# Optimization experiments

Measured on AMD Instinct MI355X. Metric: run time of the kernel, lower is better.

## Reference

```python
import jax, jax.numpy as jnp
import numpy as np
from math import lgamma, pi, sqrt

L = 20  # legendre_polys; embedding_dim = L*L = 400
SQ2 = sqrt(2.0)

def _norm(l, m):
    # K(l,m) = sqrt((2l+1)/(4pi) * (l-m)!/(l+m)!), computed stably via lgamma
    return sqrt((2 * l + 1) / (4.0 * pi)) * sqrt(np.exp(lgamma(l - m + 1) - lgamma(l + m + 1)))

def setup_inputs() -> dict:
    key = jax.random.key(0)
    k1, k2 = jax.random.split(key)
    B = 250000
    lon = jax.random.uniform(k1, (B,), minval=-180.0, maxval=180.0)
    lat = jax.random.uniform(k2, (B,), minval=-90.0, maxval=90.0)
    return {"lonlat": jnp.stack([lon, lat], axis=-1).astype(jnp.float32)}

def _sh_all(lonlat):
    # Real spherical harmonics for all (l, m), l in [0, L), m in [-l, l],
    # in the same ordering as the torch module's double loop.
    lon, lat = lonlat[:, 0], lonlat[:, 1]
    phi = jnp.deg2rad(lon + 180.0)    # azimuth in [0, 2pi)
    theta = jnp.deg2rad(lat + 90.0)   # colatitude in [0, pi]
    x = jnp.cos(theta)
    sx = jnp.sin(theta)               # = sqrt(1 - x^2) on [0, pi]

    # Associated Legendre P_l^m(x) (Condon-Shortley phase) via recurrence.
    P = {(0, 0): jnp.ones_like(x)}
    for m in range(1, L):
        P[(m, m)] = -(2 * m - 1) * sx * P[(m - 1, m - 1)]
    for m in range(L):
        if m + 1 < L:
            P[(m + 1, m)] = (2 * m + 1) * x * P[(m, m)]
        for l in range(m + 2, L):
            P[(l, m)] = ((2 * l - 1) * x * P[(l - 1, m)] - (l + m - 1) * P[(l - 2, m)]) / (l - m)

    cols = []
    for l in range(L):
        for m in range(-l, l + 1):
            am = abs(m)
            K = _norm(l, am)
            if m > 0:
                cols.append(SQ2 * K * jnp.cos(m * phi) * P[(l, m)])
            elif m < 0:
                cols.append(SQ2 * K * jnp.sin(am * phi) * P[(l, am)])
            else:
                cols.append(K * P[(l, 0)])
    return jnp.stack(cols, axis=-1)  # [B, L*L]

def reference(lonlat):
    return _sh_all(lonlat)
```

## Files before the change

kernel.cpp:

```cpp
#include <hip/hip_runtime.h>


#define L_MAX 20
#define NCOL 400
#define PTS 64
#define TPB 256
#define LSTR 205
#define SPLIT_L 14
#define C0A 0
#define CA 196
#define C0B 196
#define CB 204

constexpr double csqrt(double x) {
    double g = (x > 1.0) ? x : 1.0;
    for (int i = 0; i < 200; ++i) g = 0.5 * (g + x / g);
    return g;
}

struct CoefTbl { float c[NCOL]; };

constexpr CoefTbl make_tbl() {
    CoefTbl t{};
    const double PI  = 3.14159265358979323846;
    const double SQ2 = csqrt(2.0);
    for (int l = 0; l < L_MAX; ++l) {
        for (int m = 0; m <= l; ++m) {
            double r = 1.0;
            for (int k = l - m + 1; k <= l + m; ++k) r /= (double)k;
            double K = csqrt((2.0 * l + 1.0) / (4.0 * PI) * r);
            int base = l * l + l;
            if (m == 0) {
                t.c[base] = (float)K;
            } else {
                t.c[base + m] = (float)(SQ2 * K);
                t.c[base - m] = (float)(SQ2 * K);
            }
        }
    }
    return t;
}

static constexpr CoefTbl TBL = make_tbl();

__global__ __launch_bounds__(TPB, 3) void sh_kernel(const float2* __restrict__ lonlat,
                                                    float* __restrict__ out, int B) {
    __shared__ float tile[PTS * LSTR];

    const int tid  = threadIdx.x;
    const int lane = tid & 63;
    const int sub  = tid >> 6;
    const int blockBase = blockIdx.x * PTS;
    const int p  = blockBase + lane;
    const int pr = p < B ? p : B - 1;

    float2 ll = lonlat[pr];
    const float D2R = 0.017453292519943295f;
    float phi   = (ll.x + 180.0f) * D2R;
    float theta = (ll.y + 90.0f) * D2R;

    float x, sx, s1, c1;
    sincosf(theta, &sx, &x);
    sincosf(phi, &s1, &c1);

    float cm[L_MAX], sm[L_MAX];
    cm[0] = 1.0f; sm[0] = 0.0f;
#pragma unroll
    for (int m = 1; m < L_MAX; ++m) {
        cm[m] = cm[m - 1] * c1 - sm[m - 1] * s1;
        sm[m] = sm[m - 1] * c1 + cm[m - 1] * s1;
    }

    float Pa[L_MAX], Pb[L_MAX], Pc[L_MAX];
    float pmm = 1.0f;
    float* myrow = tile + lane * LSTR;

    auto emit = [&](int l, int c0) {
#pragma unroll
        for (int m = 0; m <= l - 2; ++m)
            Pc[m] = (float(2 * l - 1) * x * Pa[m] - float(l + m - 1) * Pb[m]) * (1.0f / float(l - m));
        if (l >= 1) {
            Pc[l - 1] = float(2 * l - 1) * x * Pa[l - 1];
            pmm = -float(2 * l - 1) * sx * pmm;
        }
        Pc[l] = pmm;

        const int gbase = l * l + l;
        const int base  = gbase - c0;
        if (sub == 0) myrow[base] = TBL.c[gbase] * Pc[0];
#pragma unroll
        for (int m = 1; m <= l; ++m) {
            if ((m & 3) == sub) {
                float t = TBL.c[gbase + m] * Pc[m];
                myrow[base + m] = t * cm[m];
                myrow[base - m] = t * sm[m];
            }
        }
#pragma unroll
        for (int m = 0; m <= l; ++m) { Pb[m] = Pa[m]; Pa[m] = Pc[m]; }
    };

#pragma unroll
    for (int l = 0; l < SPLIT_L; ++l) emit(l, C0A);

    __syncthreads();
    for (int i = tid; i < PTS * CA; i += TPB) {
        int pp = i / CA;
        int cc = i - pp * CA;
        int gp = blockBase + pp;
        if (gp < B) out[(size_t)gp * NCOL + C0A + cc] = tile[pp * LSTR + cc];
    }
    __syncthreads();

#pragma unroll
    for (int l = SPLIT_L; l < L_MAX; ++l) emit(l, C0B);

    __syncthreads();
    for (int i = tid; i < PTS * CB; i += TPB) {
        int pp = i / CB;
        int cc = i - pp * CB;
        int gp = blockBase + pp;
        if (gp < B) out[(size_t)gp * NCOL + C0B + cc] = tile[pp * LSTR + cc];
    }
}

extern "C" void kernel_launch(void* const* d_in, const int* in_sizes, int n_in,
                              void* d_out, int out_size, void* d_ws, size_t ws_size,
                              hipStream_t stream) {
    (void)n_in; (void)d_ws; (void)ws_size; (void)out_size;
    const float2* lonlat = (const float2*)d_in[0];
    float* out = (float*)d_out;
    int B = in_sizes[0] / 2;

    const int blocks = (B + PTS - 1) / PTS;
    sh_kernel<<<blocks, TPB, 0, stream>>>(lonlat, out, B);
}
```

Before: 461.5 us.

## Restructure Legendre recurrence to per-m columns owned by each sub-thread

Before, all four threads sharing a point ran the full l-major Legendre recurrence redundantly over arrays of size L and then picked out their own m values. Now the loop runs m-major: each sub-thread computes only the P_l^m columns for the m values it owns, assigned with a snake pattern to balance the work. It keeps just the scalars pm, cv and sv instead of per-m arrays. This cuts the redundant ALU work and the register pressure, at the cost of the second pass recomputing the low-l recurrence for each m.

```diff
diff --git a/kernel.cpp b/kernel.cpp
--- a/kernel.cpp
+++ b/kernel.cpp
@@ -43,6 +43,57 @@
 
 static constexpr CoefTbl TBL = make_tbl();
 
+__device__ constexpr int SUBOF[L_MAX] =
+    {0,1,2,3, 3,2,1,0, 0,1,2,3, 3,2, 1,0,0,1, 2,3};
+
+template<int L0, int L1, int C0>
+__device__ __forceinline__ void sh_pass(int sub, float x, float sx,
+                                        float c1, float s1,
+                                        float* __restrict__ myrow) {
+    constexpr int LTOP = L1 - 1;
+    float pm = 1.0f;
+    float cv = 1.0f, sv = 0.0f;
+
+    auto emit = [&](int l, int m, float p) {
+        if (l < L0) return;
+        const int g = l * l + l;
+        const int b = g - C0;
+        if (m == 0) {
+            myrow[b] = TBL.c[g] * p;
+        } else {
+            const float t = TBL.c[g + m] * p;
+            myrow[b + m] = t * cv;
+            myrow[b - m] = t * sv;
+        }
+    };
+
+#pragma unroll
+    for (int m = 0; m <= LTOP; ++m) {
+        if (SUBOF[m] == sub) {
+            float p2 = pm;
+            emit(m, m, p2);
+            if (m + 1 <= LTOP) {
+                float p1 = float(2 * m + 1) * x * p2;
+                emit(m + 1, m, p1);
+#pragma unroll
+                for (int l = m + 2; l <= LTOP; ++l) {
+                    float p0 = (float(2 * l - 1) * x * p1 -
+                                float(l + m - 1) * p2) *
+                               (1.0f / float(l - m));
+                    emit(l, m, p0);
+                    p2 = p1; p1 = p0;
+                }
+            }
+        }
+        if (m < LTOP) {
+            pm = -float(2 * m + 1) * sx * pm;
+            float cn = cv * c1 - sv * s1;
+            sv = sv * c1 + cv * s1;
+            cv = cn;
+        }
+    }
+}
+
 __global__ __launch_bounds__(TPB, 3) void sh_kernel(const float2* __restrict__ lonlat,
                                                     float* __restrict__ out, int B) {
     __shared__ float tile[PTS * LSTR];
@@ -63,45 +114,9 @@
     sincosf(theta, &sx, &x);
     sincosf(phi, &s1, &c1);
 
-    float cm[L_MAX], sm[L_MAX];
-    cm[0] = 1.0f; sm[0] = 0.0f;
-#pragma unroll
-    for (int m = 1; m < L_MAX; ++m) {
-        cm[m] = cm[m - 1] * c1 - sm[m - 1] * s1;
-        sm[m] = sm[m - 1] * c1 + cm[m - 1] * s1;
-    }
-
-    float Pa[L_MAX], Pb[L_MAX], Pc[L_MAX];
-    float pmm = 1.0f;
     float* myrow = tile + lane * LSTR;
 
-    auto emit = [&](int l, int c0) {
-#pragma unroll
-        for (int m = 0; m <= l - 2; ++m)
-            Pc[m] = (float(2 * l - 1) * x * Pa[m] - float(l + m - 1) * Pb[m]) * (1.0f / float(l - m));
-        if (l >= 1) {
-            Pc[l - 1] = float(2 * l - 1) * x * Pa[l - 1];
-            pmm = -float(2 * l - 1) * sx * pmm;
-        }
-        Pc[l] = pmm;
-
-        const int gbase = l * l + l;
-        const int base  = gbase - c0;
-        if (sub == 0) myrow[base] = TBL.c[gbase] * Pc[0];
-#pragma unroll
-        for (int m = 1; m <= l; ++m) {
-            if ((m & 3) == sub) {
-                float t = TBL.c[gbase + m] * Pc[m];
-                myrow[base + m] = t * cm[m];
-                myrow[base - m] = t * sm[m];
-            }
-        }
-#pragma unroll
-        for (int m = 0; m <= l; ++m) { Pb[m] = Pa[m]; Pa[m] = Pc[m]; }
-    };
-
-#pragma unroll
-    for (int l = 0; l < SPLIT_L; ++l) emit(l, C0A);
+    sh_pass<0, SPLIT_L, C0A>(sub, x, sx, c1, s1, myrow);
 
     __syncthreads();
     for (int i = tid; i < PTS * CA; i += TPB) {
@@ -112,8 +127,7 @@
     }
     __syncthreads();
 
-#pragma unroll
-    for (int l = SPLIT_L; l < L_MAX; ++l) emit(l, C0B);
+    sh_pass<SPLIT_L, L_MAX, C0B>(sub, x, sx, c1, s1, myrow);
 
     __syncthreads();
     for (int i = tid; i < PTS * CB; i += TPB) {
```

Measured after the change: 454.4 us. No clear change (-1.5%).
